# Kernel optimization log

Hardware: AMD Instinct MI355X
Metric: run time of the kernel (lower is better)

The kernel has to match this reference:

```python
import jax, jax.numpy as jnp
import numpy as np
from jax.scipy.special import logsumexp

EPS = 0.1
NUM_ITERS = 50
TOPO_MULT = 1.0


def _dist_cosine(x):
    # x: [N, D] -> pairwise cosine distance [N, N], clamped to >= 0
    norms = jnp.sqrt(jnp.clip(jnp.sum(x * x, axis=1, keepdims=True), 1e-8, None))
    xn = x / norms
    return jnp.clip(1.0 - xn @ xn.T, 0.0, None)


def _sinkhorn_log_domain(a, b, C):
    # a, b: [N, N] row-stochastic; C: [N, N]. Duals computed with no grad (detached).
    log_a = jnp.log(jnp.clip(a, 1e-8, None))
    log_b = jnp.log(jnp.clip(b, 1e-8, None))
    la = jax.lax.stop_gradient(log_a)
    lb = jax.lax.stop_gradient(log_b)
    lC = jax.lax.stop_gradient(-C / EPS)[None]  # [1, N, N]

    def body(i, fg):
        f, g = fg
        g = EPS * lb - EPS * logsumexp(f[:, :, None] + lC, axis=1)
        f = EPS * la - EPS * logsumexp(lC + g[:, None, :], axis=2)
        return (f, g)

    f0 = jnp.zeros_like(a)
    f, g = jax.lax.fori_loop(0, NUM_ITERS, body, (f0, f0))
    cost = jnp.sum(a * f, axis=1) + jnp.sum(b * g, axis=1)  # [N]
    return jnp.mean(cost)


def reference(x_original, x_reconstructed, z_latent, log_sigma_lat, log_var_recon, log_var_topo):
    recon_loss = jnp.mean((x_reconstructed - x_original) ** 2)

    D_orig = _dist_cosine(x_original)   # [N, N]
    D_latent = _dist_cosine(z_latent)   # [N, N]

    sigma_orig = jnp.median(D_orig)
    sigma_orig = jnp.where(sigma_orig == 0, jnp.asarray(1e-6, D_orig.dtype), sigma_orig)
    sigma_lat = jax.nn.softplus(log_sigma_lat) + 1e-6  # [1]

    S_orig = jnp.exp(-D_orig ** 2 / (2.0 * sigma_orig ** 2))
    S_lat = jnp.exp(-D_latent ** 2 / (2.0 * sigma_lat ** 2))

    N = S_orig.shape[0]
    mask = 1.0 - jnp.eye(N, dtype=S_orig.dtype)
    S_orig = S_orig * mask
    S_lat = S_lat * mask

    P_orig = S_orig / jnp.clip(jnp.sum(S_orig, axis=1, keepdims=True), 1e-8, None)
    P_lat = S_lat / jnp.clip(jnp.sum(S_lat, axis=1, keepdims=True), 1e-8, None)

    C = D_orig
    ot_orig_lat = _sinkhorn_log_domain(P_orig, P_lat, C)
    ot_lat_lat = _sinkhorn_log_domain(P_lat, P_lat, C)
    ot_orig_orig = _sinkhorn_log_domain(P_orig, P_orig, C)

    topo_loss = jnp.clip(ot_orig_lat - 0.5 * ot_lat_lat - 0.5 * ot_orig_orig, 0.0, None)
    topo_loss = topo_loss * TOPO_MULT

    prec_r = jnp.exp(-log_var_recon)  # [1]
    prec_t = jnp.exp(-log_var_topo)   # [1]
    total_loss = (0.5 * prec_r * recon_loss + 0.5 * log_var_recon
                  + 0.5 * prec_t * topo_loss + 0.5 * log_var_topo)  # [1]
    return (total_loss, recon_loss, topo_loss)


def setup_inputs() -> dict:
    key = jax.random.key(0)
    k1, k2, k3 = jax.random.split(key, 3)
    N, D, DL = 256, 4096, 256
    return {
        "x_original": jax.random.normal(k1, (N, D), dtype=jnp.float32),
        "x_reconstructed": jax.random.normal(k2, (N, D), dtype=jnp.float32),
        "z_latent": jax.random.normal(k3, (N, DL), dtype=jnp.float32),
        "log_sigma_lat": jnp.zeros((1,), dtype=jnp.float32),
        "log_var_recon": jnp.zeros((1,), dtype=jnp.float32),
        "log_var_topo": jnp.zeros((1,), dtype=jnp.float32),
    }
```

## Files before the change

kernel.cpp:

```cpp
#include <hip/hip_runtime.h>
#include <hip/hip_fp16.h>

#define EPS 0.1f
#define SINK_ITERS 50
#define KSCALE_LN 9.0109133472f
#define USTRIDE 272

typedef _Float16 f16;
typedef _Float16 f16x4 __attribute__((ext_vector_type(4)));
typedef _Float16 f16x8 __attribute__((ext_vector_type(8)));
typedef float f32x4 __attribute__((ext_vector_type(4)));

#define PIN_U4(v) asm volatile("" : "+v"(v.x), "+v"(v.y), "+v"(v.z), "+v"(v.w))

__device__ __forceinline__ float wave_red_sum(float v) {
    #pragma unroll
    for (int o = 32; o; o >>= 1) v += __shfl_xor(v, o, 64);
    return v;
}

__device__ __forceinline__ float sel4(int q, float a, float b, float c, float d) {
    float ab = (q & 1) ? b : a;
    float cd = (q & 1) ? d : c;
    return (q & 2) ? cd : ab;
}

__device__ __forceinline__ int med_bin(float v) {
    int b = (int)(v * 4096.f);
    if (v < (float)b * (1.f / 4096.f)) b--;
    else if (v >= (float)(b + 1) * (1.f / 4096.f)) b++;
    if (b < 0) b = 0;
    if (b > 8191) b = 8191;
    return b;
}

__global__ __launch_bounds__(256) void k_pre(const float4* __restrict__ xo,
                                             const float4* __restrict__ xr,
                                             const float4* __restrict__ z,
                                             f16x4* __restrict__ xh,
                                             f16x4* __restrict__ zh,
                                             float* __restrict__ rsum,
                                             float* __restrict__ acc,
                                             int* __restrict__ hist) {
    __shared__ float red[4];
    int b = blockIdx.x, t = threadIdx.x;
    if (b < 512) {
        int tid = b * 256 + t;
        float s = 0.f;
        for (int i = tid; i < 262144; i += 512 * 256) {
            float4 a = xo[i], r = xr[i];
            float d0 = r.x - a.x, d1 = r.y - a.y, d2 = r.z - a.z, d3 = r.w - a.w;
            s = fmaf(d0, d0, s); s = fmaf(d1, d1, s);
            s = fmaf(d2, d2, s); s = fmaf(d3, d3, s);
        }
        s = wave_red_sum(s);
        if ((t & 63) == 0) red[t >> 6] = s;
        __syncthreads();
        if (t == 0) rsum[b] = red[0] + red[1] + red[2] + red[3];
    } else {
        if (b < 768) {
            int row = b - 512;
            if (t < 32) hist[row * 32 + t] = 0;
            if (b == 512 && t >= 32 && t < 40) acc[t - 32] = 0.f;
        }
        int row = b - 512;
        const float4* src; f16x4* dst; int c4;
        if (row < 256) { src = xo + (size_t)row * 1024; dst = xh + (size_t)row * 1024; c4 = 1024; }
        else { src = z + (size_t)(row - 256) * 64; dst = zh + (size_t)(row - 256) * 64; c4 = 64; }
        float s = 0.f;
        for (int i = t; i < c4; i += 256) {
            float4 v = src[i];
            s = fmaf(v.x, v.x, s); s = fmaf(v.y, v.y, s);
            s = fmaf(v.z, v.z, s); s = fmaf(v.w, v.w, s);
        }
        s = wave_red_sum(s);
        if ((t & 63) == 0) red[t >> 6] = s;
        __syncthreads();
        float tot = red[0] + red[1] + red[2] + red[3];
        float rn = 1.f / sqrtf(fmaxf(tot, 1e-8f));
        for (int i = t; i < c4; i += 256) {
            float4 v = src[i];
            f16x4 h;
            h[0] = (f16)(v.x * rn); h[1] = (f16)(v.y * rn);
            h[2] = (f16)(v.z * rn); h[3] = (f16)(v.w * rn);
            dst[i] = h;
        }
    }
}

__global__ __launch_bounds__(256) void k_gemm_f16(const uint4* __restrict__ xh,
                                                  const uint4* __restrict__ zh,
                                                  float* __restrict__ part,
                                                  float* __restrict__ part2) {
    __shared__ __align__(16) f16 Ai[64 * 40], Bj[64 * 40];
    int zb = blockIdx.z;
    const uint4* X; int lda8, k0, nchunk; float* out;
    if (zb < 16) { X = xh; lda8 = 512; k0 = zb * 256; nchunk = 8; out = part + (size_t)zb * 65536; }
    else { X = zh; lda8 = 32; k0 = (zb - 16) * 64; nchunk = 2; out = part2 + (size_t)(zb - 16) * 65536; }
    int i0 = blockIdx.x * 64, j0 = blockIdx.y * 64;
    int t = threadIdx.x, lane = t & 63, wv = t >> 6;
    int m16 = lane & 15, quad = lane >> 4;
    int r = t >> 2, ko = (t & 3) * 8;
    f32x4 acc[4] = {};
    for (int ch = 0; ch < nchunk; ch++) {
        int kb8 = (k0 + ch * 32) >> 3;
        uint4 va = X[(size_t)(i0 + r) * lda8 + kb8 + (t & 3)];
        uint4 vb = X[(size_t)(j0 + r) * lda8 + kb8 + (t & 3)];
        __syncthreads();
        *(uint4*)&Ai[r * 40 + ko] = va;
        *(uint4*)&Bj[r * 40 + ko] = vb;
        __syncthreads();
        f16x8 a = *(const f16x8*)&Ai[(wv * 16 + m16) * 40 + quad * 8];
        #pragma unroll
        for (int st = 0; st < 4; st++) {
            f16x8 bfr = *(const f16x8*)&Bj[(st * 16 + m16) * 40 + quad * 8];
            acc[st] = __builtin_amdgcn_mfma_f32_16x16x32_f16(a, bfr, acc[st], 0, 0, 0);
        }
    }
    #pragma unroll
    for (int st = 0; st < 4; st++)
        #pragma unroll
        for (int reg = 0; reg < 4; reg++)
            out[(i0 + wv * 16 + quad * 4 + reg) * 256 + j0 + st * 16 + m16] = acc[st][reg];
}

__global__ __launch_bounds__(256) void k_reduce_do(const float* __restrict__ part,
                                                   float* __restrict__ Do,
                                                   int* __restrict__ hist_g) {
    int e = blockIdx.x * 256 + threadIdx.x;
    float s = 0.f;
    for (int sl = 0; sl < 16; sl++) s += part[(size_t)sl * 65536 + e];
    float v = fmaxf(1.f - s, 0.f);
    Do[e] = v;
    atomicAdd(&hist_g[med_bin(v)], 1);
}

#define MED_CAP 6144

__global__ __launch_bounds__(1024) void k_median(const float* __restrict__ D,
                                                 const int* __restrict__ hist_g,
                                                 float* __restrict__ out_sigma) {
    __shared__ float cand[MED_CAP];
    __shared__ int scan_w[16];
    __shared__ int s_cnt;
    __shared__ int s_b[2], s_r[2];
    __shared__ float s_out[2];
    int t = threadIdx.x;
    if (t == 0) s_cnt = 0;
    int h[8], loc[8];
    #pragma unroll
    for (int j = 0; j < 8; j++) h[j] = hist_g[t * 8 + j];
    int s8 = 0;
    #pragma unroll
    for (int j = 0; j < 8; j++) { loc[j] = s8; s8 += h[j]; }
    int inc = s8;
    #pragma unroll
    for (int o = 1; o < 64; o <<= 1) {
        int vv = __shfl_up(inc, o, 64);
        if ((t & 63) >= o) inc += vv;
    }
    if ((t & 63) == 63) scan_w[t >> 6] = inc;
    __syncthreads();
    int woff = 0;
    for (int wv = 0; wv < (t >> 6); wv++) woff += scan_w[wv];
    int base = woff + inc - s8;
    for (int sel = 0; sel < 2; sel++) {
        int k = 32767 + sel;
        if (base <= k && k < base + s8) {
            #pragma unroll
            for (int j = 0; j < 8; j++) {
                int lo = base + loc[j], hi = lo + h[j];
                if (lo <= k && k < hi) { s_b[sel] = t * 8 + j; s_r[sel] = k - lo; }
            }
        }
    }
    __syncthreads();
    int b0 = s_b[0], b1 = s_b[1];
    for (int i = t; i < 65536; i += 1024) {
        float v = D[i];
        int b = med_bin(v);
        if (b == b0 || b == b1) {
            int idx = atomicAdd(&s_cnt, 1);
            if (idx < MED_CAP) cand[idx] = v;
        }
    }
    __syncthreads();
    int C = s_cnt < MED_CAP ? s_cnt : MED_CAP;
    int t0 = s_r[0];
    int t1 = (b1 == b0) ? s_r[1] : (hist_g[b0] + s_r[1]);
    for (int j = t; j < C; j += 1024) {
        float vj = cand[j];
        int rk = 0;
        for (int i = 0; i < C; i++) {
            float vi = cand[i];
            rk += (vi < vj || (vi == vj && i < j)) ? 1 : 0;
        }
        if (rk == t0) s_out[0] = vj;
        if (rk == t1) s_out[1] = vj;
    }
    __syncthreads();
    if (t == 0)
        out_sigma[0] = 0.5f * (s_out[0] + s_out[1]);
}

__global__ __launch_bounds__(256) void k_prep(const float* __restrict__ Do,
                                              const float* __restrict__ part2,
                                              const float* __restrict__ wsacc,
                                              const float* __restrict__ lsl,
                                              float* __restrict__ Po, float* __restrict__ Pl,
                                              float* __restrict__ ELo, float* __restrict__ ELl,
                                              f16* __restrict__ Kh) {
    __shared__ float red[8];
    int i = blockIdx.x, j = threadIdx.x;
    int e = i * 256 + j;
    float sig_o = wsacc[4];
    if (sig_o == 0.f) sig_o = 1e-6f;
    float x = lsl[0];
    float sp = (x > 20.f) ? x : log1pf(__expf(x));
    float sig_l = sp + 1e-6f;
    float i2o = 1.f / (2.f * sig_o * sig_o);
    float i2l = 1.f / (2.f * sig_l * sig_l);
    float d_o = Do[e];
    float sD = part2[e] + part2[65536 + e] + part2[131072 + e] + part2[196608 + e];
    float d_l = fmaxf(1.f - sD, 0.f);
    float so = (i == j) ? 0.f : __expf(-d_o * d_o * i2o);
    float sl = (i == j) ? 0.f : __expf(-d_l * d_l * i2l);
    float wso = wave_red_sum(so);
    float wsl = wave_red_sum(sl);
    if ((j & 63) == 0) { red[j >> 6] = wso; red[4 + (j >> 6)] = wsl; }
    __syncthreads();
    float sum_o = red[0] + red[1] + red[2] + red[3];
    float sum_l = red[4] + red[5] + red[6] + red[7];
    float po = so / fmaxf(sum_o, 1e-8f);
    float pl = sl / fmaxf(sum_l, 1e-8f);
    Po[e] = po;
    Pl[e] = pl;
    ELo[e] = EPS * __logf(fmaxf(po, 1e-8f));
    ELl[e] = EPS * __logf(fmaxf(pl, 1e-8f));
    float kv = __expf(-d_o * (1.f / EPS) + KSCALE_LN);
    Kh[(((i >> 3) * 256 + j) << 3) + (i & 7)] = (f16)kv;
}

__global__ __launch_bounds__(256, 1) void k_sinkhorn(const float* __restrict__ Po,
                                                     const float* __restrict__ Pl,
                                                     const float* __restrict__ ELo,
                                                     const float* __restrict__ ELl,
                                                     const uint4* __restrict__ Kq,
                                                     float* __restrict__ wsacc) {
    __shared__ __align__(16) f16 U[2][4 * USTRIDE];
    __shared__ float CW[4][4];
    int t = threadIdx.x;
    int lane = t & 63, wv = t >> 6;
    int m16 = lane & 15, quad = lane >> 4;
    int w = blockIdx.x;
    int s = w >> 6;
    int ibase = (w & 63) * 4;
    int colbase = wv * 64;
    int c_lane = colbase + quad * 16 + m16;

    uint4 bf[4][8];
    #pragma unroll
    for (int ct = 0; ct < 4; ct++)
        #pragma unroll
        for (int kc = 0; kc < 8; kc++)
            bf[ct][kc] = Kq[(kc * 4 + quad) * 256 + colbase + ct * 16 + m16];
    #pragma unroll
    for (int ct = 0; ct < 4; ct++)
        #pragma unroll
        for (int kc = 0; kc < 8; kc++) PIN_U4(bf[ct][kc]);

    const float* ELa_b = (s == 1 ? ELl : ELo);
    const float* ELb_b = (s == 2 ? ELo : ELl);
    float ef[4], eg[4], Ef[4], Eg[4];
    #pragma unroll
    for (int reg = 0; reg < 4; reg++) {
        int i = ibase + reg;
        ef[reg] = ELa_b[i * 256 + c_lane] + EPS * KSCALE_LN;
        eg[reg] = ELb_b[i * 256 + c_lane] + EPS * KSCALE_LN;
        Ef[reg] = __expf(ef[reg]);
        Eg[reg] = __expf(eg[reg]);
    }

    if (t < 136)
        *(uint4*)&U[0][t * 8] =
            make_uint4(0x3C003C00u, 0x3C003C00u, 0x3C003C00u, 0x3C003C00u);
    __syncthreads();

    float zf[4], zg[4];
    for (int it = 0; it < 2 * SINK_ITERS; it++) {
        const f16* ub = &U[it & 1][0];
        f16* un = &U[(it + 1) & 1][0];
        f16x8 a[8];
        #pragma unroll
        for (int kc = 0; kc < 8; kc++)
            a[kc] = *(const f16x8*)&ub[(m16 & 3) * USTRIDE + kc * 32 + quad * 8];
        f32x4 accA[4] = {{0.f,0.f,0.f,0.f},{0.f,0.f,0.f,0.f},{0.f,0.f,0.f,0.f},{0.f,0.f,0.f,0.f}};
        f32x4 accB[4] = {{0.f,0.f,0.f,0.f},{0.f,0.f,0.f,0.f},{0.f,0.f,0.f,0.f},{0.f,0.f,0.f,0.f}};
        #pragma unroll
        for (int kc = 0; kc < 4; kc++)
            #pragma unroll
            for (int ct = 0; ct < 4; ct++)
                accA[ct] = __builtin_amdgcn_mfma_f32_16x16x32_f16(
                    a[kc], __builtin_bit_cast(f16x8, bf[ct][kc]), accA[ct], 0, 0, 0);
        #pragma unroll
        for (int kc = 4; kc < 8; kc++)
            #pragma unroll
            for (int ct = 0; ct < 4; ct++)
                accB[ct] = __builtin_amdgcn_mfma_f32_16x16x32_f16(
                    a[kc], __builtin_bit_cast(f16x8, bf[ct][kc]), accB[ct], 0, 0, 0);
        float zsum[4];
        #pragma unroll
        for (int reg = 0; reg < 4; reg++) {
            float zA = sel4(quad, accA[0][reg], accA[1][reg], accA[2][reg], accA[3][reg]);
            float zB = sel4(quad, accB[0][reg], accB[1][reg], accB[2][reg], accB[3][reg]);
            zsum[reg] = zA + zB;
        }
        if (it == 2 * SINK_ITERS - 2) {
            #pragma unroll
            for (int reg = 0; reg < 4; reg++) zg[reg] = zsum[reg];
        }
        if (it == 2 * SINK_ITERS - 1) {
            #pragma unroll
            for (int reg = 0; reg < 4; reg++) zf[reg] = zsum[reg];
        }
        bool fstep = (it & 1);
        #pragma unroll
        for (int reg = 0; reg < 4; reg++) {
            float E = fstep ? Ef[reg] : Eg[reg];
            float p = __expf(-EPS * __logf(zsum[reg]));
            un[reg * USTRIDE + c_lane] = (f16)(E * p);
        }
        __syncthreads();
    }

    const float* PaB = (s == 1 ? Pl : Po);
    const float* PbB = (s == 2 ? Po : Pl);
    float cs[4];
    #pragma unroll
    for (int reg = 0; reg < 4; reg++) {
        int i = ibase + reg;
        float dfv = ef[reg] - EPS * __logf(zf[reg]);
        float dgv = eg[reg] - EPS * __logf(zg[reg]);
        cs[reg] = PaB[i * 256 + c_lane] * dfv + PbB[i * 256 + c_lane] * dgv;
    }
    #pragma unroll
    for (int reg = 0; reg < 4; reg++) cs[reg] = wave_red_sum(cs[reg]);
    if (lane == 0) {
        #pragma unroll
        for (int reg = 0; reg < 4; reg++) CW[wv][reg] = cs[reg];
    }
    __syncthreads();
    if (t == 0) {
        float v = 0.f;
        for (int w2 = 0; w2 < 4; w2++)
            v += CW[w2][0] + CW[w2][1] + CW[w2][2] + CW[w2][3];
        atomicAdd(&wsacc[s], v);
    }
}

__global__ __launch_bounds__(512) void k_final(const float* __restrict__ rsum,
                                               const float* __restrict__ wsacc,
                                               const float* __restrict__ lvr_p,
                                               const float* __restrict__ lvt_p,
                                               float* __restrict__ out) {
    __shared__ float red[8];
    int t = threadIdx.x;
    float s = rsum[t];
    s = wave_red_sum(s);
    if ((t & 63) == 0) red[t >> 6] = s;
    __syncthreads();
    if (t == 0) {
        float rs = red[0] + red[1] + red[2] + red[3] +
                   red[4] + red[5] + red[6] + red[7];
        float recon = rs * (1.f / (256.f * 4096.f));
        float ot0 = wsacc[0] * (1.f / 256.f);
        float ot1 = wsacc[1] * (1.f / 256.f);
        float ot2 = wsacc[2] * (1.f / 256.f);
        float topo = ot0 - 0.5f * ot1 - 0.5f * ot2;
        topo = topo > 0.f ? topo : 0.f;
        float lvr = lvr_p[0], lvt = lvt_p[0];
        out[0] = 0.5f * __expf(-lvr) * recon + 0.5f * lvr +
                 0.5f * __expf(-lvt) * topo + 0.5f * lvt;
        out[1] = recon;
        out[2] = topo;
    }
}

extern "C" void kernel_launch(void* const* d_in, const int* in_sizes, int n_in,
                              void* d_out, int out_size, void* d_ws, size_t ws_size,
                              hipStream_t stream) {
    const float* xo = (const float*)d_in[0];
    const float* xr = (const float*)d_in[1];
    const float* z  = (const float*)d_in[2];
    const float* lsl = (const float*)d_in[3];
    const float* lvr = (const float*)d_in[4];
    const float* lvt = (const float*)d_in[5];
    float* out = (float*)d_out;
    float* ws = (float*)d_ws;

    float* acc  = ws;
    float* rsum = ws + 64;
    float* xh   = ws + 576;
    float* zh   = xh + 524288;
    float* Do   = zh + 32768;
    float* Po   = Do + 65536;
    float* Pl   = Po + 65536;
    float* ELo  = Pl + 65536;
    float* ELl  = ELo + 65536;
    float* Kh   = ELl + 65536;
    float* part = Kh + 32768;
    int*   hist = (int*)(part + 1048576);
    float* part2 = Po;

    k_pre<<<1024, 256, 0, stream>>>((const float4*)xo, (const float4*)xr, (const float4*)z,
                                    (f16x4*)xh, (f16x4*)zh, rsum, acc, hist);
    k_gemm_f16<<<dim3(4, 4, 20), 256, 0, stream>>>((const uint4*)xh, (const uint4*)zh,
                                                   part, part2);
    k_reduce_do<<<256, 256, 0, stream>>>(part, Do, hist);
    k_median<<<1, 1024, 0, stream>>>(Do, hist, acc + 4);
    k_prep<<<256, 256, 0, stream>>>(Do, part2, acc, lsl, Po, Pl, ELo, ELl, (f16*)Kh);
    k_sinkhorn<<<192, 256, 0, stream>>>(Po, Pl, ELo, ELl, (const uint4*)Kh, acc);
    k_final<<<1, 512, 0, stream>>>(rsum, acc, lvr, lvt, out);
}
```

Measured before the change: 236.7 us.

## Fuse Do reduction with median and final reduction into sinkhorn via last-block tickets

Merges the partial-sum reduction kernel and the single-block median kernel into one kernel, where the last block to arrive (tracked by an atomic ticket counter) computes the median. The final loss kernel is folded into the sinkhorn kernel the same way, using a second ticket. This cuts two kernel launches and their inter-kernel gaps, at the cost of threadfence and atomic counter overhead. The median candidate scan also switches to float4 loads.

```diff
diff --git a/kernel.cpp b/kernel.cpp
--- a/kernel.cpp
+++ b/kernel.cpp
@@ -61,7 +61,7 @@
         if (b < 768) {
             int row = b - 512;
             if (t < 32) hist[row * 32 + t] = 0;
-            if (b == 512 && t >= 32 && t < 40) acc[t - 32] = 0.f;
+            if (b == 512 && t >= 32 && t < 48) acc[t - 32] = 0.f;
         }
         int row = b - 512;
         const float4* src; f16x4* dst; int c4;
@@ -124,29 +124,36 @@
             out[(i0 + wv * 16 + quad * 4 + reg) * 256 + j0 + st * 16 + m16] = acc[st][reg];
 }
 
-__global__ __launch_bounds__(256) void k_reduce_do(const float* __restrict__ part,
-                                                   float* __restrict__ Do,
-                                                   int* __restrict__ hist_g) {
-    int e = blockIdx.x * 256 + threadIdx.x;
-    float s = 0.f;
-    for (int sl = 0; sl < 16; sl++) s += part[(size_t)sl * 65536 + e];
-    float v = fmaxf(1.f - s, 0.f);
-    Do[e] = v;
-    atomicAdd(&hist_g[med_bin(v)], 1);
-}
-
 #define MED_CAP 6144
 
-__global__ __launch_bounds__(1024) void k_median(const float* __restrict__ D,
-                                                 const int* __restrict__ hist_g,
+__global__ __launch_bounds__(1024) void k_do_med(const float* __restrict__ part,
+                                                 float* __restrict__ Do,
+                                                 int* __restrict__ hist_g,
+                                                 int* __restrict__ tick,
                                                  float* __restrict__ out_sigma) {
     __shared__ float cand[MED_CAP];
     __shared__ int scan_w[16];
     __shared__ int s_cnt;
     __shared__ int s_b[2], s_r[2];
     __shared__ float s_out[2];
+    __shared__ int amLast;
     int t = threadIdx.x;
-    if (t == 0) s_cnt = 0;
+    int e = blockIdx.x * 1024 + t;
+    {
+        float s = 0.f;
+        for (int sl = 0; sl < 16; sl++) s += part[(size_t)sl * 65536 + e];
+        float v = fmaxf(1.f - s, 0.f);
+        Do[e] = v;
+        atomicAdd(&hist_g[med_bin(v)], 1);
+    }
+    __threadfence();
+    if (t == 0) {
+        amLast = (atomicAdd(tick, 1) == 63);
+        s_cnt = 0;
+    }
+    __syncthreads();
+    if (!amLast) return;
+
     int h[8], loc[8];
     #pragma unroll
     for (int j = 0; j < 8; j++) h[j] = hist_g[t * 8 + j];
@@ -176,12 +183,17 @@
     }
     __syncthreads();
     int b0 = s_b[0], b1 = s_b[1];
-    for (int i = t; i < 65536; i += 1024) {
-        float v = D[i];
-        int b = med_bin(v);
-        if (b == b0 || b == b1) {
-            int idx = atomicAdd(&s_cnt, 1);
-            if (idx < MED_CAP) cand[idx] = v;
+    const float4* D4 = (const float4*)Do;
+    for (int i = t; i < 16384; i += 1024) {
+        float4 v4 = D4[i];
+        float vv[4] = {v4.x, v4.y, v4.z, v4.w};
+        #pragma unroll
+        for (int q = 0; q < 4; q++) {
+            int b = med_bin(vv[q]);
+            if (b == b0 || b == b1) {
+                int idx = atomicAdd(&s_cnt, 1);
+                if (idx < MED_CAP) cand[idx] = vv[q];
+            }
         }
     }
     __syncthreads();
@@ -246,9 +258,16 @@
                                                      const float* __restrict__ ELo,
                                                      const float* __restrict__ ELl,
                                                      const uint4* __restrict__ Kq,
-                                                     float* __restrict__ wsacc) {
+                                                     float* __restrict__ wsacc,
+                                                     int* __restrict__ tick,
+                                                     const float* __restrict__ rsum,
+                                                     const float* __restrict__ lvr_p,
+                                                     const float* __restrict__ lvt_p,
+                                                     float* __restrict__ out) {
     __shared__ __align__(16) f16 U[2][4 * USTRIDE];
     __shared__ float CW[4][4];
+    __shared__ float fred[8];
+    __shared__ int amLast;
     int t = threadIdx.x;
     int lane = t & 63, wv = t >> 6;
     int m16 = lane & 15, quad = lane >> 4;
@@ -355,23 +374,18 @@
         for (int w2 = 0; w2 < 4; w2++)
             v += CW[w2][0] + CW[w2][1] + CW[w2][2] + CW[w2][3];
         atomicAdd(&wsacc[s], v);
-    }
-}
-
-__global__ __launch_bounds__(512) void k_final(const float* __restrict__ rsum,
-                                               const float* __restrict__ wsacc,
-                                               const float* __restrict__ lvr_p,
-                                               const float* __restrict__ lvt_p,
-                                               float* __restrict__ out) {
-    __shared__ float red[8];
-    int t = threadIdx.x;
-    float s = rsum[t];
-    s = wave_red_sum(s);
-    if ((t & 63) == 0) red[t >> 6] = s;
+        __threadfence();
+        amLast = (atomicAdd(tick, 1) == 191);
+    }
+    __syncthreads();
+    if (!amLast) return;
+
+    float r2 = rsum[t] + rsum[t + 256];
+    r2 = wave_red_sum(r2);
+    if ((t & 63) == 0) fred[t >> 6] = r2;
     __syncthreads();
     if (t == 0) {
-        float rs = red[0] + red[1] + red[2] + red[3] +
-                   red[4] + red[5] + red[6] + red[7];
+        float rs = fred[0] + fred[1] + fred[2] + fred[3];
         float recon = rs * (1.f / (256.f * 4096.f));
         float ot0 = wsacc[0] * (1.f / 256.f);
         float ot1 = wsacc[1] * (1.f / 256.f);
@@ -416,9 +430,8 @@
                                     (f16x4*)xh, (f16x4*)zh, rsum, acc, hist);
     k_gemm_f16<<<dim3(4, 4, 20), 256, 0, stream>>>((const uint4*)xh, (const uint4*)zh,
                                                    part, part2);
-    k_reduce_do<<<256, 256, 0, stream>>>(part, Do, hist);
-    k_median<<<1, 1024, 0, stream>>>(Do, hist, acc + 4);
+    k_do_med<<<64, 1024, 0, stream>>>(part, Do, hist, (int*)(acc + 8), acc + 4);
     k_prep<<<256, 256, 0, stream>>>(Do, part2, acc, lsl, Po, Pl, ELo, ELl, (f16*)Kh);
-    k_sinkhorn<<<192, 256, 0, stream>>>(Po, Pl, ELo, ELl, (const uint4*)Kh, acc);
-    k_final<<<1, 512, 0, stream>>>(rsum, acc, lvr, lvt, out);
-}
+    k_sinkhorn<<<192, 256, 0, stream>>>(Po, Pl, ELo, ELl, (const uint4*)Kh, acc,
+                                        (int*)(acc + 9), rsum, lvr, lvt, out);
+}
```

Result: faster. 229.6 us (-3.0%).
